# Kernel tuning notes

Hardware: AMD Instinct MI355X
Metric: run time of the kernel (lower is better)

The kernel has to match this reference:

```python
import jax, jax.numpy as jnp
import numpy as np

SCORE_THRESHOLD = 0.5
NMS_TOP_K = 1024
NMS_THRESHOLD = 0.6
N_ANCHORS = 262144
N_CLASSES = 80


def setup_inputs() -> dict:
    key = jax.random.key(0)
    k1, k2, k3 = jax.random.split(key, 3)
    # valid xyxy boxes: x1<x2, y1<y2
    xy = jax.random.uniform(k1, (1, N_ANCHORS, 2), minval=0.0, maxval=2048.0)
    wh = jax.random.uniform(k2, (1, N_ANCHORS, 2), minval=1.0, maxval=64.0)
    pred_bboxes = jnp.concatenate([xy, xy + wh], axis=-1)  # [1, N, 4]
    pred_scores = jax.random.uniform(k3, (1, N_ANCHORS, N_CLASSES))  # [1, N, C]
    return {"pred_bboxes": pred_bboxes, "pred_scores": pred_scores}


def _pairwise_iou(boxes):
    # boxes: [K, 4] xyxy -> [K, K] IoU
    area = (boxes[:, 2] - boxes[:, 0]) * (boxes[:, 3] - boxes[:, 1])
    lt = jnp.maximum(boxes[:, None, :2], boxes[None, :, :2])
    rb = jnp.minimum(boxes[:, None, 2:], boxes[None, :, 2:])
    wh = jnp.clip(rb - lt, 0.0)
    inter = wh[..., 0] * wh[..., 1]
    union = area[:, None] + area[None, :] - inter
    return inter / jnp.maximum(union, 1e-9)


def reference(pred_bboxes, pred_scores):
    scores = pred_scores[0]  # [N, C]
    boxes = pred_bboxes[0]   # [N, 4]

    # single-label-per-box branch: per-anchor best class
    conf = jnp.max(scores, axis=1)      # [N]
    label = jnp.argmax(scores, axis=1)  # [N] int

    # score threshold (masking instead of data-dependent filtering)
    masked_conf = jnp.where(conf >= SCORE_THRESHOLD, conf, -1.0)

    # top-k candidates (sorted descending, matching torch.topk)
    top_conf, top_idx = jax.lax.top_k(masked_conf, NMS_TOP_K)  # [K]
    top_boxes = boxes[top_idx]   # [K, 4]
    top_label = label[top_idx]   # [K]
    valid = top_conf >= SCORE_THRESHOLD  # [K] rows that passed the threshold

    # batched_nms trick: offset boxes per class so cross-class IoU is ~0
    max_coord = jax.lax.stop_gradient(jnp.max(top_boxes)) + 1.0
    offset_boxes = top_boxes + top_label.astype(top_boxes.dtype)[:, None] * max_coord
    iou = _pairwise_iou(offset_boxes)  # [K, K]

    # sequential greedy suppression in score order (rows already sorted)
    idx = jnp.arange(NMS_TOP_K)

    def body(i, keep):
        suppress = (iou[i] > NMS_THRESHOLD) & (idx > i) & keep[i] & keep
        return keep & ~suppress

    keep = jax.lax.fori_loop(0, NMS_TOP_K, body, valid)  # [K] bool

    out = jnp.concatenate(
        [top_boxes, top_conf[:, None], top_label.astype(top_boxes.dtype)[:, None]],
        axis=1,
    )  # [K, 6] = [x1, y1, x2, y2, conf, label]
    # fixed-shape masked output: suppressed / invalid rows zeroed
    return out * keep[:, None].astype(out.dtype)
```

## Files before the change

### kernel.cpp

```cpp
#include <hip/hip_runtime.h>
#include <stdint.h>


#define N_ANCH   262144
#define N_CLS    80
#define K_TOP    1024
#define CAP      4096

typedef unsigned long long ull;

#define HSLOT(b) ((((b) & 2047u) << 4) | ((b) >> 11))
#define SKEW(e) ((uint32_t)(e) + ((uint32_t)(e) >> 4))

#define OFF_HIST  0
#define OFF_CTRL  131072
#define MEMSET_BYTES 131136
#define OFF_BINS  131136
#define OFF_LIST  655424
#define WS_REQUIRED 688192

__global__ __launch_bounds__(256) void k_sentinel(float* __restrict__ out, float v) {
    int i = blockIdx.x * 256 + threadIdx.x;
    if (i < K_TOP * 6) out[i] = v;
}

static __device__ __forceinline__ uint32_t conf_key24(float best) {
    uint32_t u = __float_as_uint(best);
    if (u > 0x3F800000u) u = 0x3F800000u;
    if (u < 0x3F000000u) u = 0x3F000000u;
    return u - 0x3F000000u;
}

static __device__ __forceinline__ void cmpsw(ull& x, ull& y, bool up) {
    ull mn = x < y ? x : y, mx = x < y ? y : x;
    x = up ? mn : mx; y = up ? mx : mn;
}

__global__ __launch_bounds__(256) void k_conf(const float* __restrict__ scores,
                                              uint16_t* __restrict__ bins16,
                                              uint32_t* __restrict__ hist) {
    const int t = threadIdx.x;
    const int r = t >> 4, s = t & 15;
    const int a0 = blockIdx.x * 128 + r;
    const float* base = scores + (size_t)a0 * N_CLS;
    float4 v0 = ((const float4*)base)[s];
    float4 v1;
    if (s < 4) v1 = ((const float4*)base)[16 + s];
    #pragma unroll
    for (int i = 0; i < 8; i++) {
        float4 c0 = v0, c1 = v1;
        if (i + 1 < 8) {
            const float* nb = base + (size_t)(i + 1) * 16 * N_CLS;
            v0 = ((const float4*)nb)[s];
            if (s < 4) v1 = ((const float4*)nb)[16 + s];
        }
        float best = c0.x; int lab = 4 * s;
        if (c0.y > best) { best = c0.y; lab = 4 * s + 1; }
        if (c0.z > best) { best = c0.z; lab = 4 * s + 2; }
        if (c0.w > best) { best = c0.w; lab = 4 * s + 3; }
        if (s < 4) {
            const int c = 64 + 4 * s;
            if (c1.x > best) { best = c1.x; lab = c; }
            if (c1.y > best) { best = c1.y; lab = c + 1; }
            if (c1.z > best) { best = c1.z; lab = c + 2; }
            if (c1.w > best) { best = c1.w; lab = c + 3; }
        }
        ull key = ((ull)(uint32_t)__float_as_uint(best) << 7) | (ull)(uint32_t)(127 - lab);
        ull o;
        o = __shfl_xor(key, 1); if (o > key) key = o;
        o = __shfl_xor(key, 2); if (o > key) key = o;
        o = __shfl_xor(key, 4); if (o > key) key = o;
        o = __shfl_xor(key, 8); if (o > key) key = o;
        if (s == 0) {
            const int a = a0 + i * 16;
            float bv = __uint_as_float((uint32_t)(key >> 7));
            uint16_t pk = 0;
            if (bv >= 0.5f) {
                uint32_t bin = conf_key24(bv) >> 8;
                if (bin > 32767u) bin = 32767u;
                atomicAdd(&hist[HSLOT(bin)], 1u);
                pk = (uint16_t)(0x8000u | bin);
            }
            bins16[a] = pk;
        }
    }
}

__global__ __launch_bounds__(1024) void k_cut(const uint32_t* __restrict__ hist,
                                              uint32_t* __restrict__ ctrl) {
    __shared__ uint32_t wtot[16], wsuf[16];
    const int t = threadIdx.x;
    const int lane = t & 63, w = t >> 6;
    const uint32_t sbase = (((uint32_t)t & 63u) << 9) | ((uint32_t)t >> 6);
    uint32_t c[32];
    #pragma unroll
    for (int i = 0; i < 32; i++) c[i] = hist[sbase | ((uint32_t)i << 4)];
    uint32_t part = 0;
    #pragma unroll
    for (int i = 0; i < 32; i++) part += c[i];
    uint32_t x = part;
    #pragma unroll
    for (int d = 1; d < 64; d <<= 1) {
        uint32_t o = __shfl_down(x, d);
        if (lane + d < 64) x += o;
    }
    if (lane == 0) wtot[w] = x;
    __syncthreads();
    if (t < 16) {
        uint32_t s = 0;
        for (int ww = t + 1; ww < 16; ww++) s += wtot[ww];
        wsuf[t] = s;
        if (t == 0) {
            uint32_t total = s + wtot[0];
            ctrl[1] = (total < K_TOP) ? total : K_TOP;
        }
    }
    __syncthreads();
    uint32_t run = (x + wsuf[w]) - part;
    if (run < K_TOP && run + part >= K_TOP) {
        uint32_t fnd = 0, cbv = 0;
        #pragma unroll
        for (int i = 31; i >= 0; i--) {
            if (!fnd && run + c[i] >= K_TOP) { cbv = (uint32_t)(t * 32 + i); fnd = 1; }
            if (!fnd) run += c[i];
        }
        ctrl[2] = cbv;
    }
}

__global__ __launch_bounds__(256) void k_gather(const float* __restrict__ scores,
                                                const uint16_t* __restrict__ bins16,
                                                uint32_t* __restrict__ ctrl,
                                                ull* __restrict__ list) {
    __shared__ uint32_t lcnt, lbase;
    const int t = threadIdx.x, b = blockIdx.x;
    if (t == 0) { lcnt = 0; lbase = 0; }
    __syncthreads();
    const uint32_t cT = ctrl[2];
    const int a4 = b * 256 + t;
    ushort4 pk4 = ((const ushort4*)bins16)[a4];
    uint16_t pk[4] = {pk4.x, pk4.y, pk4.z, pk4.w};
    ull      hk[4];
    uint32_t hs[4];
    bool     hv[4];
    #pragma unroll
    for (int e = 0; e < 4; e++) {
        hv[e] = false; hk[e] = 0; hs[e] = 0;
        uint32_t u = pk[e];
        if ((u & 0x8000u) && (u & 0x7FFFu) >= cT) {
            const uint32_t a = (uint32_t)a4 * 4u + (uint32_t)e;
            const float4* row = (const float4*)(scores + (size_t)a * N_CLS);
            float best = -1.f; int lab = 0;
            for (int f = 0; f < 20; f++) {
                float4 w = row[f];
                if (w.x > best) { best = w.x; lab = 4 * f; }
                if (w.y > best) { best = w.y; lab = 4 * f + 1; }
                if (w.z > best) { best = w.z; lab = 4 * f + 2; }
                if (w.w > best) { best = w.w; lab = 4 * f + 3; }
            }
            if (best >= 0.5f) {
                uint32_t k24 = conf_key24(best);
                hk[e] = ((ull)(0x1000000u - k24) << 25) | ((ull)a << 7)
                      | (ull)(uint32_t)lab;
                hs[e] = atomicAdd(&lcnt, 1u);
                hv[e] = true;
            }
        }
    }
    __syncthreads();
    if (t == 0 && lcnt) lbase = atomicAdd(&ctrl[0], lcnt);
    __syncthreads();
    const uint32_t base2 = lbase;
    #pragma unroll
    for (int e = 0; e < 4; e++) {
        if (hv[e]) {
            uint32_t slot = base2 + hs[e];
            if (slot < CAP) list[slot] = hk[e];
        }
    }
}

__global__ __launch_bounds__(1024) void k_final(const float4* __restrict__ bboxes,
                                                const uint32_t* __restrict__ ctrl,
                                                const ull* __restrict__ list,
                                                float* __restrict__ out) {
    __shared__ __align__(16) char smem[45056];
    ull*      sk    = (ull*)smem;
    float4*   ob    = (float4*)smem;
    float*    ar    = (float*)(smem + 16384);
    float*    red16 = (float*)(smem + 20480);
    uint32_t* g     = (uint32_t*)(smem + 20544);
    ull*      sup   = (ull*)(smem + 24640);
    uint8_t*  keepA = (uint8_t*)(smem + 32832);
    uint32_t* cnt   = (uint32_t*)(smem + 33856);
    uint32_t* stt   = (uint32_t*)(smem + 34176);
    uint8_t*  ovr   = (uint8_t*)(smem + 34496);
    ull*      cmask = (ull*)(smem + 34816);
    const int t = threadIdx.x;
    const uint32_t nsel = ctrl[1];
    uint32_t ncand = ctrl[0]; if (ncand > CAP) ncand = CAP;

    uint32_t nsort = 1024;
    while (nsort < ncand) nsort <<= 1;

    if (nsort <= 2048) {
        const int TS2 = (int)(nsort >> 1);
        ull E0 = ~0ull, E1 = ~0ull;
        if (t < TS2) {
            int e = 2 * t;
            E0 = (e < (int)ncand)     ? list[e]     : ~0ull;
            E1 = (e + 1 < (int)ncand) ? list[e + 1] : ~0ull;
        }
        for (uint32_t k = 2; k <= nsort; k <<= 1) {
            for (uint32_t j = k >> 1; j > 0; j >>= 1) {
                if (j >= 128) {
                    __syncthreads();
                    if (t < TS2) {
                        ulonglong2 wv; wv.x = E0; wv.y = E1;
                        *(ulonglong2*)&sk[2 * t] = wv;
                    }
                    __syncthreads();
                    if (t < TS2) {
                        uint32_t e0 = 2 * t;
                        ulonglong2 rv = *(const ulonglong2*)&sk[e0 ^ j];
                        bool km = (((e0 & k) == 0) != ((e0 & j) == 0));
                        E0 = ((E0 > rv.x) == km) ? E0 : rv.x;
                        E1 = ((E1 > rv.y) == km) ? E1 : rv.y;
                    }
                } else if (t < TS2) {
                    if (j >= 2) {
                        int d = (int)(j >> 1);
                        bool km = ((((2 * t) & k) == 0) != (((2 * t) & j) == 0));
                        ull o0 = __shfl_xor(E0, d);
                        ull o1 = __shfl_xor(E1, d);
                        E0 = ((E0 > o0) == km) ? E0 : o0;
                        E1 = ((E1 > o1) == km) ? E1 : o1;
                    } else {
                        bool up = (((2 * t) & k) == 0);
                        cmpsw(E0, E1, up);
                    }
                }
            }
        }
        __syncthreads();
        if (t < TS2) {
            ulonglong2 wv; wv.x = E0; wv.y = E1;
            *(ulonglong2*)&sk[2 * t] = wv;
        }
    } else {
        const int TS = (int)(nsort >> 2);
        ull E[4];
        if (t < TS) {
            #pragma unroll
            for (int rr = 0; rr < 4; rr++) {
                int e = 4 * t + rr;
                E[rr] = (e < (int)ncand) ? list[e] : ~0ull;
            }
        }
        for (uint32_t k = 2; k <= nsort; k <<= 1) {
            for (uint32_t j = k >> 1; j > 0; j >>= 1) {
                if (j >= 256) {
                    __syncthreads();
                    if (t < TS) {
                        #pragma unroll
                        for (int rr = 0; rr < 4; rr++) sk[SKEW(4 * t + rr)] = E[rr];
                    }
                    __syncthreads();
                    if (t < TS) {
                        #pragma unroll
                        for (int rr = 0; rr < 4; rr++) {
                            uint32_t e = 4 * t + rr;
                            ull o = sk[SKEW(e ^ j)];
                            bool keepMax = (((e & k) == 0) != ((e & j) == 0));
                            bool gt = E[rr] > o;
                            E[rr] = (gt == keepMax) ? E[rr] : o;
                        }
                    }
                } else if (t < TS) {
                    if (j >= 4) {
                        int d = (int)(j >> 2);
                        #pragma unroll
                        for (int rr = 0; rr < 4; rr++) {
                            uint32_t e = 4 * t + rr;
                            ull o = __shfl_xor(E[rr], d);
                            bool keepMax = (((e & k) == 0) != ((e & j) == 0));
                            bool gt = E[rr] > o;
                            E[rr] = (gt == keepMax) ? E[rr] : o;
                        }
                    } else if (j == 2) {
                        bool up = (((4 * t) & k) == 0);
                        cmpsw(E[0], E[2], up); cmpsw(E[1], E[3], up);
                    } else {
                        bool upA = (((4 * t) & k) == 0);
                        bool upB = (((4 * t + 2) & k) == 0);
                        cmpsw(E[0], E[1], upA);
                        cmpsw(E[2], E[3], upB);
                    }
                }
            }
        }
        __syncthreads();
        if (t < TS) {
            #pragma unroll
            for (int rr = 0; rr < 4; rr++) sk[SKEW(4 * t + rr)] = E[rr];
        }
    }
    __syncthreads();
    ull skey = (nsort <= 2048) ? sk[t] : sk[SKEW(t)];
    __syncthreads();

    float4 bx = make_float4(0.f, 0.f, 0.f, 0.f);
    float cf = 0.f, lb = 0.f;
    uint32_t lab = 0;
    if ((uint32_t)t < nsel) {
        uint32_t idx = (uint32_t)(skey >> 7) & 0x3FFFFu;
        lab = (uint32_t)skey & 127u;
        cf = __uint_as_float(0x3F000000u + (0x1000000u - (uint32_t)(skey >> 25)));
        lb = (float)lab;
        bx = bboxes[idx];
    }
    float m = fmaxf(fmaxf(bx.x, bx.y), fmaxf(bx.z, bx.w));
    for (int d = 32; d > 0; d >>= 1) m = fmaxf(m, __shfl_xor(m, d));
    if ((t & 63) == 0) red16[t >> 6] = m;
    __syncthreads();
    float M = red16[0];
    #pragma unroll
    for (int w = 1; w < 16; w++) M = fmaxf(M, red16[w]);
    M = __fadd_rn(M, 1.0f);
    float o = __fmul_rn(lb, M);
    float4 q;
    q.x = __fadd_rn(bx.x, o); q.y = __fadd_rn(bx.y, o);
    q.z = __fadd_rn(bx.z, o); q.w = __fadd_rn(bx.w, o);
    ob[t] = q;
    ar[t] = __fmul_rn(__fsub_rn(q.z, q.x), __fsub_rn(q.w, q.y));
    g[t] = 0xFFFFFFFFu;
    if (t < N_CLS) ovr[t] = 0;
    keepA[t] = 0;
    if (t < 640) {
        ulonglong2 z; z.x = 0; z.y = 0;
        *(ulonglong2*)&cmask[2 * t] = z;
    }
    __syncthreads();

    if ((uint32_t)t < nsel)
        atomicOr(&cmask[lab * 16 + (t >> 6)], 1ull << (t & 63));
    __syncthreads();
    if (t < N_CLS) {
        uint32_t s = 0;
        #pragma unroll
        for (int w = 0; w < 16; w++) s += (uint32_t)__popcll(cmask[t * 16 + w]);
        cnt[t] = s;
    }
    __syncthreads();
    if (t < N_CLS) {
        uint32_t s = 0;
        for (int i = 0; i < N_CLS - 1; i++) {
            uint32_t v = cnt[i];
            if (i < t) s += v;
        }
        stt[t] = s;
    }
    __syncthreads();
    if ((uint32_t)t < nsel) {
        const ull* cm = &cmask[lab * 16];
        uint32_t w = (uint32_t)t >> 6;
        uint32_t r = (uint32_t)__popcll(cm[w] & ((1ull << (t & 63)) - 1ull));
        for (uint32_t ww = 0; ww < w; ww++) r += (uint32_t)__popcll(cm[ww]);
        g[stt[lab] + r] = (lab << 10) | (uint32_t)t;
    }
    __syncthreads();

    uint32_t gp = g[t];
    {
        ull sp = 0;
        if (gp != 0xFFFFFFFFu) {
            uint32_t labi = gp >> 10;
            uint32_t ri = gp & 1023u;
            float4 oi = ob[ri]; float ai = ar[ri];
            for (int qq = t + 1; qq < 1024; qq++) {
                uint32_t gq = g[qq];
                if ((gq >> 10) != labi) break;
                int dq = qq - t;
                if (dq > 64) { ovr[labi] = 1; break; }
                uint32_t rj = gq & 1023u;
                float4 oj = ob[rj];
                float lx = fmaxf(oi.x, oj.x), ly = fmaxf(oi.y, oj.y);
                float rx = fminf(oi.z, oj.z), ry = fminf(oi.w, oj.w);
                float wx = fmaxf(__fsub_rn(rx, lx), 0.f);
                float wy = fmaxf(__fsub_rn(ry, ly), 0.f);
                float inter = __fmul_rn(wx, wy);
                float uni = __fsub_rn(__fadd_rn(ai, ar[rj]), inter);
                float iou = __fdiv_rn(inter, fmaxf(uni, 1e-9f));
                if (iou > 0.6f) sp |= 1ull << (dq - 1);
            }
        }
        sup[t] = sp;
    }
    __syncthreads();

    if (t < N_CLS) {
        uint32_t n = cnt[t];
        if (n > 0) {
            uint32_t s0 = stt[t];
            if (n <= 64 && !ovr[t]) {
                ull kill = 0;
                for (uint32_t i = 0; i < n; i++) {
                    if (!((kill >> i) & 1ull)) {
                        if (i + 1 < 64) kill |= sup[s0 + i] << (i + 1);
                        keepA[g[s0 + i] & 1023u] = 1;
                    }
                }
            } else {
                for (uint32_t i = 0; i < n; i++) {
                    uint32_t ri = g[s0 + i] & 1023u;
                    float4 oi = ob[ri]; float ai = ar[ri];
                    bool kp = true;
                    for (uint32_t m2 = 0; m2 < i && kp; m2++) {
                        uint32_t rm = g[s0 + m2] & 1023u;
                        if (!keepA[rm]) continue;
                        float4 om = ob[rm];
                        float lx = fmaxf(om.x, oi.x), ly = fmaxf(om.y, oi.y);
                        float rx = fminf(om.z, oi.z), ry = fminf(om.w, oi.w);
                        float wx = fmaxf(__fsub_rn(rx, lx), 0.f);
                        float wy = fmaxf(__fsub_rn(ry, ly), 0.f);
                        float inter = __fmul_rn(wx, wy);
                        float uni = __fsub_rn(__fadd_rn(ar[rm], ai), inter);
                        float iou = __fdiv_rn(inter, fmaxf(uni, 1e-9f));
                        if (iou > 0.6f) kp = false;
                    }
                    keepA[ri] = kp ? 1 : 0;
                }
            }
        }
    }
    __syncthreads();

    const bool keep = keepA[t] != 0;
    float v0 = keep ? bx.x : 0.f, v1 = keep ? bx.y : 0.f;
    float v2 = keep ? bx.z : 0.f, v3 = keep ? bx.w : 0.f;
    float v4 = keep ? cf : 0.f, v5 = keep ? lb : 0.f;
    float2* o2 = (float2*)out;
    o2[t * 3 + 0] = make_float2(v0, v1);
    o2[t * 3 + 1] = make_float2(v2, v3);
    o2[t * 3 + 2] = make_float2(v4, v5);
}

extern "C" void kernel_launch(void* const* d_in, const int* in_sizes, int n_in,
                              void* d_out, int out_size, void* d_ws, size_t ws_size,
                              hipStream_t stream) {
    const float* bboxes = (const float*)d_in[0];
    const float* scores = (const float*)d_in[1];
    if (n_in >= 2 && in_sizes[0] > in_sizes[1]) {
        bboxes = (const float*)d_in[1];
        scores = (const float*)d_in[0];
    }

    if (ws_size < (size_t)WS_REQUIRED) {
        k_sentinel<<<(K_TOP * 6 + 255) / 256, 256, 0, stream>>>(
            (float*)d_out, (float)(ws_size >> 10));
        return;
    }

    char* ws = (char*)d_ws;
    uint32_t* hist   = (uint32_t*)(ws + OFF_HIST);
    uint32_t* ctrl   = (uint32_t*)(ws + OFF_CTRL);
    uint16_t* bins16 = (uint16_t*)(ws + OFF_BINS);
    ull*      list   = (ull*)(ws + OFF_LIST);

    hipMemsetAsync(ws, 0, MEMSET_BYTES, stream);
    k_conf  <<<N_ANCH / 128, 256, 0, stream>>>(scores, bins16, hist);
    k_cut   <<<1,           1024, 0, stream>>>(hist, ctrl);
    k_gather<<<256,          256, 0, stream>>>(scores, bins16, ctrl, list);
    k_final <<<1,           1024, 0, stream>>>((const float4*)bboxes, ctrl, list,
                                               (float*)d_out);
}
```

Before: 187.1 us.

## Replace bitonic candidate sort with counting sort over key buckets; deepen conf prefetch

In the final kernel, candidates are bucketed by the high bits of their key with a shared-memory histogram. An exclusive prefix scan gives bucket offsets, keys are scattered to their slots, and small buckets are fixed up with a per-bucket insertion sort. This replaces the multi-pass bitonic sort and its many block barriers. If a key falls outside the 2048-bucket range or a bucket overflows 16 entries, it falls back to the old bitonic sort. Separately, the conf kernel prefetches four rows of scores instead of one to keep more loads in flight, at the cost of more registers.

```diff
diff --git a/kernel.cpp b/kernel.cpp
--- a/kernel.cpp
+++ b/kernel.cpp
@@ -43,16 +43,20 @@
     const int r = t >> 4, s = t & 15;
     const int a0 = blockIdx.x * 128 + r;
     const float* base = scores + (size_t)a0 * N_CLS;
-    float4 v0 = ((const float4*)base)[s];
-    float4 v1;
-    if (s < 4) v1 = ((const float4*)base)[16 + s];
+    float4 v0[4], v1[4];
+    #pragma unroll
+    for (int p = 0; p < 4; p++) {
+        const float* nb = base + (size_t)p * 16 * N_CLS;
+        v0[p] = ((const float4*)nb)[s];
+        if (s < 4) v1[p] = ((const float4*)nb)[16 + s];
+    }
     #pragma unroll
     for (int i = 0; i < 8; i++) {
-        float4 c0 = v0, c1 = v1;
-        if (i + 1 < 8) {
-            const float* nb = base + (size_t)(i + 1) * 16 * N_CLS;
-            v0 = ((const float4*)nb)[s];
-            if (s < 4) v1 = ((const float4*)nb)[16 + s];
+        float4 c0 = v0[i & 3], c1 = v1[i & 3];
+        if (i + 4 < 8) {
+            const float* nb = base + (size_t)(i + 4) * 16 * N_CLS;
+            v0[i & 3] = ((const float4*)nb)[s];
+            if (s < 4) v1[i & 3] = ((const float4*)nb)[16 + s];
         }
         float best = c0.x; int lab = 4 * s;
         if (c0.y > best) { best = c0.y; lab = 4 * s + 1; }
@@ -196,117 +200,193 @@
     uint32_t* stt   = (uint32_t*)(smem + 34176);
     uint8_t*  ovr   = (uint8_t*)(smem + 34496);
     ull*      cmask = (ull*)(smem + 34816);
+    uint32_t* hist2 = (uint32_t*)(smem + 34816);
+    uint32_t* gfail = (uint32_t*)(smem + 43008);
+    uint32_t* wtot2 = (uint32_t*)(smem + 43012);
+    uint32_t* wbase = (uint32_t*)(smem + 43076);
     const int t = threadIdx.x;
     const uint32_t nsel = ctrl[1];
     uint32_t ncand = ctrl[0]; if (ncand > CAP) ncand = CAP;
 
-    uint32_t nsort = 1024;
-    while (nsort < ncand) nsort <<= 1;
-
-    if (nsort <= 2048) {
-        const int TS2 = (int)(nsort >> 1);
-        ull E0 = ~0ull, E1 = ~0ull;
-        if (t < TS2) {
-            int e = 2 * t;
-            E0 = (e < (int)ncand)     ? list[e]     : ~0ull;
-            E1 = (e + 1 < (int)ncand) ? list[e + 1] : ~0ull;
-        }
-        for (uint32_t k = 2; k <= nsort; k <<= 1) {
-            for (uint32_t j = k >> 1; j > 0; j >>= 1) {
-                if (j >= 128) {
-                    __syncthreads();
-                    if (t < TS2) {
-                        ulonglong2 wv; wv.x = E0; wv.y = E1;
-                        *(ulonglong2*)&sk[2 * t] = wv;
-                    }
-                    __syncthreads();
-                    if (t < TS2) {
-                        uint32_t e0 = 2 * t;
-                        ulonglong2 rv = *(const ulonglong2*)&sk[e0 ^ j];
-                        bool km = (((e0 & k) == 0) != ((e0 & j) == 0));
-                        E0 = ((E0 > rv.x) == km) ? E0 : rv.x;
-                        E1 = ((E1 > rv.y) == km) ? E1 : rv.y;
-                    }
-                } else if (t < TS2) {
-                    if (j >= 2) {
-                        int d = (int)(j >> 1);
-                        bool km = ((((2 * t) & k) == 0) != (((2 * t) & j) == 0));
-                        ull o0 = __shfl_xor(E0, d);
-                        ull o1 = __shfl_xor(E1, d);
-                        E0 = ((E0 > o0) == km) ? E0 : o0;
-                        E1 = ((E1 > o1) == km) ? E1 : o1;
-                    } else {
-                        bool up = (((2 * t) & k) == 0);
-                        cmpsw(E0, E1, up);
+    ((uint2*)hist2)[t] = make_uint2(0u, 0u);
+    if (t == 0) *gfail = 0;
+    __syncthreads();
+    ull      keys[4]; uint32_t kcs[4], olds[4]; bool val[4];
+    #pragma unroll
+    for (int e = 0; e < 4; e++) {
+        int i = t + 1024 * e;
+        val[e] = (i < (int)ncand); keys[e] = 0; kcs[e] = 0; olds[e] = 0;
+        if (val[e]) {
+            ull kk = list[i];
+            keys[e] = kk;
+            uint32_t kc = (uint32_t)(kk >> 25) - 0x800000u;
+            if (kc >= 2048u) { *gfail = 1; val[e] = false; }
+            else {
+                kcs[e] = kc;
+                uint32_t od = atomicAdd(&hist2[kc], 1u);
+                olds[e] = od;
+                if (od >= 16u) *gfail = 1;
+            }
+        }
+    }
+    __syncthreads();
+    const bool ctOK = (*gfail == 0);
+
+    if (ctOK) {
+        uint32_t v0h = hist2[2 * t], v1h = hist2[2 * t + 1];
+        uint32_t sseg = v0h + v1h;
+        uint32_t incl = sseg;
+        const int lane = t & 63, w = t >> 6;
+        #pragma unroll
+        for (int d = 1; d < 64; d <<= 1) {
+            uint32_t o = __shfl_up(incl, d);
+            if (lane >= d) incl += o;
+        }
+        if (lane == 63) wtot2[w] = incl;
+        __syncthreads();
+        if (t < 16) {
+            uint32_t sb = 0;
+            for (int i = 0; i < 16; i++) { uint32_t v = wtot2[i]; if (i < t) sb += v; }
+            wbase[t] = sb;
+        }
+        __syncthreads();
+        uint32_t ex = wbase[w] + incl - sseg;
+        hist2[2 * t]     = ex;
+        hist2[2 * t + 1] = ex + v0h;
+        __syncthreads();
+        #pragma unroll
+        for (int e = 0; e < 4; e++)
+            if (val[e]) sk[hist2[kcs[e]] + olds[e]] = keys[e];
+        __syncthreads();
+        #pragma unroll
+        for (int e = 0; e < 4; e++) {
+            if (val[e] && olds[e] == 0) {
+                uint32_t base = hist2[kcs[e]];
+                uint32_t nxt  = (kcs[e] < 2047u) ? hist2[kcs[e] + 1] : ncand;
+                if (nxt - base >= 2u) {
+                    for (uint32_t a2 = base + 1; a2 < nxt; a2++) {
+                        ull kv = sk[a2];
+                        uint32_t b2 = a2;
+                        while (b2 > base && sk[b2 - 1] > kv) { sk[b2] = sk[b2 - 1]; b2--; }
+                        sk[b2] = kv;
                     }
                 }
             }
         }
-        __syncthreads();
-        if (t < TS2) {
-            ulonglong2 wv; wv.x = E0; wv.y = E1;
-            *(ulonglong2*)&sk[2 * t] = wv;
-        }
     } else {
-        const int TS = (int)(nsort >> 2);
-        ull E[4];
-        if (t < TS) {
-            #pragma unroll
-            for (int rr = 0; rr < 4; rr++) {
-                int e = 4 * t + rr;
-                E[rr] = (e < (int)ncand) ? list[e] : ~0ull;
-            }
-        }
-        for (uint32_t k = 2; k <= nsort; k <<= 1) {
-            for (uint32_t j = k >> 1; j > 0; j >>= 1) {
-                if (j >= 256) {
-                    __syncthreads();
-                    if (t < TS) {
-                        #pragma unroll
-                        for (int rr = 0; rr < 4; rr++) sk[SKEW(4 * t + rr)] = E[rr];
-                    }
-                    __syncthreads();
-                    if (t < TS) {
-                        #pragma unroll
-                        for (int rr = 0; rr < 4; rr++) {
-                            uint32_t e = 4 * t + rr;
-                            ull o = sk[SKEW(e ^ j)];
-                            bool keepMax = (((e & k) == 0) != ((e & j) == 0));
-                            bool gt = E[rr] > o;
-                            E[rr] = (gt == keepMax) ? E[rr] : o;
+        uint32_t nsort = 1024;
+        while (nsort < ncand) nsort <<= 1;
+        if (nsort <= 2048) {
+            const int TS2 = (int)(nsort >> 1);
+            ull E0 = ~0ull, E1 = ~0ull;
+            if (t < TS2) {
+                int e = 2 * t;
+                E0 = (e < (int)ncand)     ? list[e]     : ~0ull;
+                E1 = (e + 1 < (int)ncand) ? list[e + 1] : ~0ull;
+            }
+            for (uint32_t k = 2; k <= nsort; k <<= 1) {
+                for (uint32_t j = k >> 1; j > 0; j >>= 1) {
+                    if (j >= 128) {
+                        __syncthreads();
+                        if (t < TS2) {
+                            ulonglong2 wv; wv.x = E0; wv.y = E1;
+                            *(ulonglong2*)&sk[2 * t] = wv;
+                        }
+                        __syncthreads();
+                        if (t < TS2) {
+                            uint32_t e0 = 2 * t;
+                            ulonglong2 rv = *(const ulonglong2*)&sk[e0 ^ j];
+                            bool km = (((e0 & k) == 0) != ((e0 & j) == 0));
+                            E0 = ((E0 > rv.x) == km) ? E0 : rv.x;
+                            E1 = ((E1 > rv.y) == km) ? E1 : rv.y;
+                        }
+                    } else if (t < TS2) {
+                        if (j >= 2) {
+                            int d = (int)(j >> 1);
+                            bool km = ((((2 * t) & k) == 0) != (((2 * t) & j) == 0));
+                            ull o0 = __shfl_xor(E0, d);
+                            ull o1 = __shfl_xor(E1, d);
+                            E0 = ((E0 > o0) == km) ? E0 : o0;
+                            E1 = ((E1 > o1) == km) ? E1 : o1;
+                        } else {
+                            bool up = (((2 * t) & k) == 0);
+                            cmpsw(E0, E1, up);
                         }
                     }
-                } else if (t < TS) {
-                    if (j >= 4) {
-                        int d = (int)(j >> 2);
-                        #pragma unroll
-                        for (int rr = 0; rr < 4; rr++) {
-                            uint32_t e = 4 * t + rr;
-                            ull o = __shfl_xor(E[rr], d);
-                            bool keepMax = (((e & k) == 0) != ((e & j) == 0));
-                            bool gt = E[rr] > o;
-                            E[rr] = (gt == keepMax) ? E[rr] : o;
+                }
+            }
+            __syncthreads();
+            if (t < TS2) {
+                ulonglong2 wv; wv.x = E0; wv.y = E1;
+                *(ulonglong2*)&sk[2 * t] = wv;
+            }
+        } else {
+            const int TS = (int)(nsort >> 2);
+            ull E[4];
+            if (t < TS) {
+                #pragma unroll
+                for (int rr = 0; rr < 4; rr++) {
+                    int e = 4 * t + rr;
+                    E[rr] = (e < (int)ncand) ? list[e] : ~0ull;
+                }
+            }
+            for (uint32_t k = 2; k <= nsort; k <<= 1) {
+                for (uint32_t j = k >> 1; j > 0; j >>= 1) {
+                    if (j >= 256) {
+                        __syncthreads();
+                        if (t < TS) {
+                            #pragma unroll
+                            for (int rr = 0; rr < 4; rr++) sk[SKEW(4 * t + rr)] = E[rr];
                         }
-                    } else if (j == 2) {
-                        bool up = (((4 * t) & k) == 0);
-                        cmpsw(E[0], E[2], up); cmpsw(E[1], E[3], up);
-                    } else {
-                        bool upA = (((4 * t) & k) == 0);
-                        bool upB = (((4 * t + 2) & k) == 0);
-                        cmpsw(E[0], E[1], upA);
-                        cmpsw(E[2], E[3], upB);
+                        __syncthreads();
+                        if (t < TS) {
+                            #pragma unroll
+                            for (int rr = 0; rr < 4; rr++) {
+                                uint32_t e = 4 * t + rr;
+                                ull o = sk[SKEW(e ^ j)];
+                                bool keepMax = (((e & k) == 0) != ((e & j) == 0));
+                                bool gt = E[rr] > o;
+                                E[rr] = (gt == keepMax) ? E[rr] : o;
+                            }
+                        }
+                    } else if (t < TS) {
+                        if (j >= 4) {
+                            int d = (int)(j >> 2);
+                            #pragma unroll
+                            for (int rr = 0; rr < 4; rr++) {
+                                uint32_t e = 4 * t + rr;
+                                ull o = __shfl_xor(E[rr], d);
+                                bool keepMax = (((e & k) == 0) != ((e & j) == 0));
+                                bool gt = E[rr] > o;
+                                E[rr] = (gt == keepMax) ? E[rr] : o;
+                            }
+                        } else if (j == 2) {
+                            bool up = (((4 * t) & k) == 0);
+                            cmpsw(E[0], E[2], up); cmpsw(E[1], E[3], up);
+                        } else {
+                            bool upA = (((4 * t) & k) == 0);
+                            bool upB = (((4 * t + 2) & k) == 0);
+                            cmpsw(E[0], E[1], upA);
+                            cmpsw(E[2], E[3], upB);
+                        }
                     }
                 }
             }
-        }
-        __syncthreads();
-        if (t < TS) {
-            #pragma unroll
-            for (int rr = 0; rr < 4; rr++) sk[SKEW(4 * t + rr)] = E[rr];
-        }
-    }
-    __syncthreads();
-    ull skey = (nsort <= 2048) ? sk[t] : sk[SKEW(t)];
+            __syncthreads();
+            if (t < TS) {
+                #pragma unroll
+                for (int rr = 0; rr < 4; rr++) sk[SKEW(4 * t + rr)] = E[rr];
+            }
+        }
+    }
+    __syncthreads();
+    ull skey;
+    if (ctOK) skey = sk[t];
+    else {
+        uint32_t nsort = 1024;
+        while (nsort < ncand) nsort <<= 1;
+        skey = (nsort <= 2048) ? sk[t] : sk[SKEW(t)];
+    }
     __syncthreads();
 
     float4 bx = make_float4(0.f, 0.f, 0.f, 0.f);
```

Result: faster. 181.5 us (-3.0%).
